# Performance work log

Hardware: AMD Instinct MI355X
Metric: run time of the kernel (lower is better)

Reference implementation:

```python
import jax, jax.numpy as jnp
import numpy as np

B, S, E, H, L, F, V = 8, 1024, 768, 12, 6, 3072, 32000
HD = E // H  # head_dim = 64
EPS = 1e-5


def _pos_encoding(max_len, dim):
    pos = np.arange(max_len, dtype=np.float32)[:, None]
    div = np.exp(np.arange(0, dim, 2, dtype=np.float32) * (-np.log(10000.0) / dim))
    pe = np.zeros((max_len, dim), dtype=np.float32)
    pe[:, 0::2] = np.sin(pos * div)
    pe[:, 1::2] = np.cos(pos * div)
    return jnp.asarray(pe)


def setup_inputs() -> dict:
    key = jax.random.key(0)
    ks = jax.random.split(key, 16)
    sd = 0.02
    inp = {}
    inp['input_ids'] = jax.random.randint(ks[0], (B, S), 0, V)
    inp['attention_mask'] = jnp.ones((B, S), dtype=jnp.int32)
    inp['emb'] = jax.random.normal(ks[1], (V, E), jnp.float32) * sd
    inp['pe'] = _pos_encoding(S, E)
    inp['Wq'] = jax.random.normal(ks[2], (L, E, E), jnp.float32) * sd
    inp['bq'] = jnp.zeros((L, E), jnp.float32)
    inp['Wk'] = jax.random.normal(ks[3], (L, E, E), jnp.float32) * sd
    inp['bk'] = jnp.zeros((L, E), jnp.float32)
    inp['Wv'] = jax.random.normal(ks[4], (L, E, E), jnp.float32) * sd
    inp['bv'] = jnp.zeros((L, E), jnp.float32)
    inp['Wo'] = jax.random.normal(ks[5], (L, E, E), jnp.float32) * sd
    inp['bo'] = jnp.zeros((L, E), jnp.float32)
    inp['ln1_g'] = jnp.ones((L, E), jnp.float32)
    inp['ln1_b'] = jnp.zeros((L, E), jnp.float32)
    inp['W1'] = jax.random.normal(ks[6], (L, E, F), jnp.float32) * sd
    inp['b1'] = jnp.zeros((L, F), jnp.float32)
    inp['W2'] = jax.random.normal(ks[7], (L, F, E), jnp.float32) * sd
    inp['b2'] = jnp.zeros((L, E), jnp.float32)
    inp['ln2_g'] = jnp.ones((L, E), jnp.float32)
    inp['ln2_b'] = jnp.zeros((L, E), jnp.float32)
    inp['Wc'] = jax.random.normal(ks[8], (E, 2), jnp.float32) * sd
    inp['bc'] = jnp.zeros((2,), jnp.float32)
    return inp


def _layernorm(x, g, b):
    mu = jnp.mean(x, axis=-1, keepdims=True)
    var = jnp.mean(jnp.square(x - mu), axis=-1, keepdims=True)
    return (x - mu) * jax.lax.rsqrt(var + EPS) * g + b


def reference(input_ids, attention_mask, emb, pe, Wq, bq, Wk, bk, Wv, bv, Wo, bo,
              ln1_g, ln1_b, W1, b1, W2, b2, ln2_g, ln2_b, Wc, bc):
    x = emb[input_ids] + pe[None, :S, :]           # [B,S,E] (dropout = eval identity)
    mask = attention_mask[:, None, None, :]        # [B,1,1,S]
    scale = jnp.sqrt(jnp.float32(HD))

    def block(x, p):
        wq, bq_, wk, bk_, wv, bv_, wo, bo_, g1, be1, w1, b1_, w2, b2_, g2, be2 = p
        q = (x @ wq + bq_).reshape(B, S, H, HD).transpose(0, 2, 1, 3)  # [B,H,S,D]
        k = (x @ wk + bk_).reshape(B, S, H, HD).transpose(0, 2, 1, 3)
        v = (x @ wv + bv_).reshape(B, S, H, HD).transpose(0, 2, 1, 3)
        scores = jnp.einsum('bhsd,bhtd->bhst', q, k) / scale          # [B,H,S,S]
        scores = jnp.where(mask == 0, -jnp.inf, scores)
        attn = jax.nn.softmax(scores, axis=-1)
        o = jnp.einsum('bhst,bhtd->bhsd', attn, v)
        o = o.transpose(0, 2, 1, 3).reshape(B, S, E) @ wo + bo_
        x = _layernorm(x + o, g1, be1)
        ffn = jax.nn.relu(x @ w1 + b1_) @ w2 + b2_
        x = _layernorm(x + ffn, g2, be2)
        return x, None

    params = (Wq, bq, Wk, bk, Wv, bv, Wo, bo, ln1_g, ln1_b, W1, b1, W2, b2, ln2_g, ln2_b)
    x, _ = jax.lax.scan(block, x, params)
    pooled = jnp.mean(x, axis=1)                   # [B,E]
    return pooled @ Wc + bc                        # [B,2]
```

## Files before the change

### kernel.cpp

```cpp
#include <hip/hip_runtime.h>

typedef __bf16 bf16x8 __attribute__((ext_vector_type(8)));
typedef float  f32x4  __attribute__((ext_vector_type(4)));

constexpr int Bb = 8, Ss = 1024, Ee = 768, Hh = 12, Ll = 6, Ff = 3072;
constexpr int TOK  = Bb * Ss;
constexpr int NQKV = 3 * Ee;

static __device__ __forceinline__ f32x4 mfma16(bf16x8 a, bf16x8 b, f32x4 c) {
  return __builtin_amdgcn_mfma_f32_16x16x32_bf16(a, b, c, 0, 0, 0);
}

static __device__ __forceinline__ void async16(const void* g, void* l) {
  __builtin_amdgcn_global_load_lds(
      (const __attribute__((address_space(1))) unsigned int*)g,
      (__attribute__((address_space(3))) unsigned int*)l, 16, 0, 0);
}

static __device__ __forceinline__ bf16x8 ds_read128(const __bf16* p) {
  bf16x8 r;
  unsigned a = (unsigned)(size_t)p;
  asm volatile("ds_read_b128 %0, %1" : "=v"(r) : "v"(a));
  return r;
}

static __device__ __forceinline__ float fexp2(float x) {
  float r; asm("v_exp_f32 %0, %1" : "=v"(r) : "v"(x)); return r;
}

__global__ __launch_bounds__(256) void embed_kernel(
    const int* __restrict__ ids, const float* __restrict__ emb,
    const float* __restrict__ pe, float* __restrict__ x, __bf16* __restrict__ xb)
{
  int tok = blockIdx.x;
  int s   = tok & (Ss - 1);
  int id  = ids[tok];
  const float* er = emb + (size_t)id * Ee;
  const float* pr = pe  + (size_t)s  * Ee;
  size_t base = (size_t)tok * Ee;
#pragma unroll
  for (int i = 0; i < 3; i++) {
    int e = threadIdx.x + i * 256;
    float v = er[e] + pr[e];
    x[base + e]  = v;
    xb[base + e] = (__bf16)v;
  }
}

__global__ __launch_bounds__(256) void transpose_w_kernel(
    const float* __restrict__ src, __bf16* __restrict__ dst,
    int K, int N, size_t sls, size_t dls)
{
  __shared__ float t[32][33];
  src += (size_t)blockIdx.z * sls;
  dst += (size_t)blockIdx.z * dls;
  int n0 = blockIdx.x * 32, k0 = blockIdx.y * 32;
  int c = threadIdx.x & 31, r0 = threadIdx.x >> 5;
#pragma unroll
  for (int rr = 0; rr < 32; rr += 8)
    t[r0 + rr][c] = src[(size_t)(k0 + r0 + rr) * N + n0 + c];
  __syncthreads();
#pragma unroll
  for (int rr = 0; rr < 32; rr += 8)
    dst[(size_t)(n0 + r0 + rr) * K + k0 + c] = (__bf16)t[c][r0 + rr];
}

template<bool OUT_BF16, bool RELU>
__global__ __launch_bounds__(256, 3) void gemm_kernel(
    const __bf16* __restrict__ A, const __bf16* __restrict__ Bt,
    const float* __restrict__ bias0, const float* __restrict__ bias1,
    const float* __restrict__ bias2, int bseg,
    float* __restrict__ Cf, __bf16* __restrict__ Cb, int M, int N, int K)
{
  __shared__ __align__(16) __bf16 lA[3][64 * 64];
  __shared__ __align__(16) __bf16 lB[3][64 * 64];
  const int tid  = threadIdx.x;
  const int wave = tid >> 6, lane = tid & 63;
  const int quad = lane >> 4, c16 = lane & 15;
  const int wm = wave >> 1, wn = wave & 1;

  const int bid = blockIdx.x;
  const int xcd = bid & 7;
  const int lb  = bid >> 3;
  const int mb  = xcd * 8 + (lb & 7);
  const int nb  = lb >> 3;
  const size_t m0 = (size_t)mb * 128, n0 = (size_t)nb * 128;

  f32x4 acc[4][4] = {};

  const int s0l = tid >> 3;
  const int s0c = tid & 7;
  const int l0  = s0c ^ (s0l & 7);
  const int tr0 = (s0l << 1) | (l0 >> 2);
  const int gc0 = (l0 & 3) * 8;
  const int s1l = (tid + 256) >> 3;
  const int l1  = s0c ^ (s1l & 7);
  const int tr1 = (s1l << 1) | (l1 >> 2);
  const int gc1 = (l1 & 3) * 8;

  const __bf16* Ag0 = A  + (m0 + tr0) * K + gc0;
  const __bf16* Ag1 = A  + (m0 + tr1) * K + gc1;
  const __bf16* Bg0 = Bt + (n0 + tr0) * K + gc0;
  const __bf16* Bg1 = Bt + (n0 + tr1) * K + gc1;
  const int d0 = tid * 8;

  const int nk = K >> 5;

  auto stage = [&](int t, int slot) {
    const int kof = t << 5;
    async16(Ag0 + kof, &lA[slot][d0]);
    async16(Ag1 + kof, &lA[slot][d0 + 2048]);
    async16(Bg0 + kof, &lB[slot][d0]);
    async16(Bg1 + kof, &lB[slot][d0 + 2048]);
  };

  int aoff[4], boff[4];
#pragma unroll
  for (int f = 0; f < 4; f++) {
    int ra = wm * 64 + f * 16 + c16;
    int ja = ra >> 1;
    aoff[f] = ja * 64 + (((((ra & 1) << 2) | quad)) ^ (ja & 7)) * 8;
    int rb = wn * 64 + f * 16 + c16;
    int jb = rb >> 1;
    boff[f] = jb * 64 + (((((rb & 1) << 2) | quad)) ^ (jb & 7)) * 8;
  }

  stage(0, 0);
  stage(1, 1);
  asm volatile("s_waitcnt vmcnt(4)" ::: "memory");
  __builtin_amdgcn_s_barrier();
  __builtin_amdgcn_sched_barrier(0);

  int slot = 0;
  for (int t = 0; t < nk; ++t) {
    if (t + 2 < nk) {
      int ns = slot + 2; if (ns >= 3) ns -= 3;
      stage(t + 2, ns);
    }
    const __bf16* la = &lA[slot][0];
    const __bf16* lb = &lB[slot][0];
    bf16x8 af[4], bfr[4];
#pragma unroll
    for (int f = 0; f < 4; f++) af[f]  = ds_read128(la + aoff[f]);
#pragma unroll
    for (int f = 0; f < 4; f++) bfr[f] = ds_read128(lb + boff[f]);
    asm volatile("s_waitcnt lgkmcnt(0)" ::: "memory");
    __builtin_amdgcn_sched_barrier(0);
    __builtin_amdgcn_s_setprio(1);
#pragma unroll
    for (int mi = 0; mi < 4; mi++)
#pragma unroll
      for (int ni = 0; ni < 4; ni++)
        acc[mi][ni] = mfma16(af[mi], bfr[ni], acc[mi][ni]);
    __builtin_amdgcn_s_setprio(0);
    __builtin_amdgcn_sched_barrier(0);
    if (t + 2 < nk) asm volatile("s_waitcnt vmcnt(4)" ::: "memory");
    else            asm volatile("s_waitcnt vmcnt(0)" ::: "memory");
    __builtin_amdgcn_s_barrier();
    __builtin_amdgcn_sched_barrier(0);
    slot = (slot + 1 == 3) ? 0 : slot + 1;
  }

#pragma unroll
  for (int ni = 0; ni < 4; ni++) {
    int col = (int)n0 + wn * 64 + ni * 16 + c16;
    const float* bp = bias0;
    int cc = col;
    if (cc >= bseg) { bp = bias1; cc -= bseg; }
    if (cc >= bseg) { bp = bias2; cc -= bseg; }
    float bv = bp[cc];
#pragma unroll
    for (int mi = 0; mi < 4; mi++) {
#pragma unroll
      for (int rr = 0; rr < 4; rr++) {
        size_t row = m0 + wm * 64 + mi * 16 + quad * 4 + rr;
        float v = acc[mi][ni][rr] + bv;
        if (RELU) v = fmaxf(v, 0.f);
        if (OUT_BF16) Cb[row * N + col] = (__bf16)v;
        else          Cf[row * N + col] = v;
      }
    }
  }
}

template<bool RELU>
__global__ __launch_bounds__(256, 2) void gemm_big_kernel(
    const __bf16* __restrict__ A, const __bf16* __restrict__ Bt,
    const float* __restrict__ bias0, const float* __restrict__ bias1,
    const float* __restrict__ bias2, int bseg,
    __bf16* __restrict__ Cb, int N, int K)
{
  __shared__ __align__(16) __bf16 lA[3][128 * 64];
  __shared__ __align__(16) __bf16 lB[3][64 * 64];
  const int tid  = threadIdx.x;
  const int wave = tid >> 6, lane = tid & 63;
  const int quad = lane >> 4, c16 = lane & 15;
  const int wm = wave >> 1, wn = wave & 1;

  const int bid = blockIdx.x;
  const int xcd = bid & 7;
  const int lb  = bid >> 3;
  const int mb  = xcd * 4 + (lb & 3);
  const int nb  = lb >> 2;
  const size_t m0 = (size_t)mb * 256, n0 = (size_t)nb * 128;

  f32x4 acc[8][4] = {};

  const __bf16* Agp[4];
#pragma unroll
  for (int j = 0; j < 4; j++) {
    int s = tid + j * 256, lr = s >> 3, sc = s & 7;
    int l = sc ^ (lr & 7);
    int tr = (lr << 1) | (l >> 2), gc = (l & 3) * 8;
    Agp[j] = A + (m0 + tr) * (size_t)K + gc;
  }
  const __bf16* Bgp[2];
#pragma unroll
  for (int j = 0; j < 2; j++) {
    int s = tid + j * 256, lr = s >> 3, sc = s & 7;
    int l = sc ^ (lr & 7);
    int tr = (lr << 1) | (l >> 2), gc = (l & 3) * 8;
    Bgp[j] = Bt + (n0 + tr) * (size_t)K + gc;
  }
  const int d0 = tid * 8;

  const int nk = K >> 5;

  auto stage = [&](int t, int slot) {
    const int kof = t << 5;
#pragma unroll
    for (int j = 0; j < 4; j++)
      async16(Agp[j] + kof, &lA[slot][d0 + j * 2048]);
#pragma unroll
    for (int j = 0; j < 2; j++)
      async16(Bgp[j] + kof, &lB[slot][d0 + j * 2048]);
  };

  int aoff[8], boff[4];
#pragma unroll
  for (int f = 0; f < 8; f++) {
    int ra = wm * 128 + f * 16 + c16;
    int ja = ra >> 1;
    aoff[f] = ja * 64 + ((((ra & 1) << 2) | quad) ^ (ja & 7)) * 8;
  }
#pragma unroll
  for (int f = 0; f < 4; f++) {
    int rb = wn * 64 + f * 16 + c16;
    int jb = rb >> 1;
    boff[f] = jb * 64 + ((((rb & 1) << 2) | quad) ^ (jb & 7)) * 8;
  }

  stage(0, 0);
  stage(1, 1);
  asm volatile("s_waitcnt vmcnt(6)" ::: "memory");
  __builtin_amdgcn_s_barrier();
  __builtin_amdgcn_sched_barrier(0);

  int slot = 0;
  for (int t = 0; t < nk; ++t) {
    if (t + 2 < nk) {
      int ns = slot + 2; if (ns >= 3) ns -= 3;
      stage(t + 2, ns);
    }
    const __bf16* la  = &lA[slot][0];
    const __bf16* lbp = &lB[slot][0];
    bf16x8 af[8], bfr[4];
#pragma unroll
    for (int f = 0; f < 8; f++) af[f]  = ds_read128(la + aoff[f]);
#pragma unroll
    for (int f = 0; f < 4; f++) bfr[f] = ds_read128(lbp + boff[f]);
    asm volatile("s_waitcnt lgkmcnt(0)" ::: "memory");
    __builtin_amdgcn_sched_barrier(0);
    __builtin_amdgcn_s_setprio(1);
#pragma unroll
    for (int mi = 0; mi < 8; mi++)
#pragma unroll
      for (int ni = 0; ni < 4; ni++)
        acc[mi][ni] = mfma16(af[mi], bfr[ni], acc[mi][ni]);
    __builtin_amdgcn_s_setprio(0);
    __builtin_amdgcn_sched_barrier(0);
    if (t + 2 < nk) asm volatile("s_waitcnt vmcnt(6)" ::: "memory");
    else            asm volatile("s_waitcnt vmcnt(0)" ::: "memory");
    __builtin_amdgcn_s_barrier();
    __builtin_amdgcn_sched_barrier(0);
    slot = (slot + 1 == 3) ? 0 : slot + 1;
  }

#pragma unroll
  for (int ni = 0; ni < 4; ni++) {
    int col = (int)n0 + wn * 64 + ni * 16 + c16;
    const float* bp = bias0;
    int cc = col;
    if (cc >= bseg) { bp = bias1; cc -= bseg; }
    if (cc >= bseg) { bp = bias2; cc -= bseg; }
    float bv = bp[cc];
#pragma unroll
    for (int mi = 0; mi < 8; mi++) {
#pragma unroll
      for (int rr = 0; rr < 4; rr++) {
        size_t row = m0 + wm * 128 + mi * 16 + quad * 4 + rr;
        float v = acc[mi][ni][rr] + bv;
        if (RELU) v = fmaxf(v, 0.f);
        Cb[row * N + col] = (__bf16)v;
      }
    }
  }
}

__global__ __launch_bounds__(256) void vtrans_kernel(
    const __bf16* __restrict__ qkv, __bf16* __restrict__ vt)
{
  int tid  = blockIdx.x * 256 + threadIdx.x;
  int d    = tid & 63;
  int rest = tid >> 6;
  int sc   = rest & 127;
  int bh   = rest >> 7;
  int b = bh / Hh, h = bh % Hh;
  const __bf16* src = qkv + (size_t)(b * Ss + sc * 8) * NQKV + 2 * Ee + h * 64 + d;
  bf16x8 v;
#pragma unroll
  for (int i = 0; i < 8; i++) v[i] = src[(size_t)i * NQKV];
  *(bf16x8*)(vt + ((size_t)bh * 64 + d) * Ss + sc * 8) = v;
}

__global__ __launch_bounds__(512, 6) void attn_kernel(
    const __bf16* __restrict__ qkv, const __bf16* __restrict__ vt,
    const int* __restrict__ amask, __bf16* __restrict__ out)
{
  __shared__ __align__(16) __bf16 kbuf[2][64 * 64];
  __shared__ __align__(16) __bf16 vbuf[2][64 * 64];
  __shared__ __align__(16) __bf16 plds[8][16 * 68];
  const int idx = blockIdx.x;
  const int bh = idx % 96, qi = idx / 96;
  const int b = bh / Hh, h = bh % Hh;
  const int lane = threadIdx.x & 63, wave = threadIdx.x >> 6;
  const int quad = lane >> 4, c16 = lane & 15;
  const int q0 = qi * 128 + wave * 16;

  const __bf16* qbase = qkv + (size_t)(b * Ss + q0 + c16) * NQKV + h * 64 + quad * 8;
  bf16x8 qf0 = *(const bf16x8*)(qbase);
  bf16x8 qf1 = *(const bf16x8*)(qbase + 32);

  const int srow = threadIdx.x >> 3;
  const int scol = ((threadIdx.x & 7) ^ (srow & 7)) * 8;
  const __bf16* kg = qkv + (size_t)(b * Ss + srow) * NQKV + Ee + h * 64 + scol;
  const __bf16* vg = vt + ((size_t)bh * 64 + srow) * Ss + scol;

  const int sa8 = c16 & 7;
  const int rc0 = (quad ^ sa8) * 8;
  const int rc1 = ((quad + 4) ^ sa8) * 8;

  f32x4 o[4] = {};
  float lrow[4] = {0.f, 0.f, 0.f, 0.f};
  const int* mp = amask + b * Ss;
  __bf16* pw = &plds[wave][0];
  const float CE = 0.18033688f;

  async16(kg, &kbuf[0][(size_t)threadIdx.x * 8]);
  async16(vg, &vbuf[0][(size_t)threadIdx.x * 8]);

  for (int t = 0; t < 16; t++) {
    const int tb = t * 64;
    __syncthreads();
    if (t < 15) {
      const int nb = (t + 1) & 1, ntb = tb + 64;
      async16(kg + (size_t)ntb * NQKV, &kbuf[nb][(size_t)threadIdx.x * 8]);
      async16(vg + ntb,                &vbuf[nb][(size_t)threadIdx.x * 8]);
    }
    const __bf16* kb = &kbuf[t & 1][0];
    const __bf16* vb = &vbuf[t & 1][0];

    float mk2[4];
#pragma unroll
    for (int n = 0; n < 4; n++) mk2[n] = mp[tb + n * 16 + c16] ? 0.f : -1e30f;
    bf16x8 kf[8], vf[8];
#pragma unroll
    for (int n = 0; n < 4; n++) {
      kf[2*n]   = *(const bf16x8*)(kb + (n * 16 + c16) * 64 + rc0);
      kf[2*n+1] = *(const bf16x8*)(kb + (n * 16 + c16) * 64 + rc1);
    }
#pragma unroll
    for (int n = 0; n < 4; n++) {
      vf[2*n]   = *(const bf16x8*)(vb + (n * 16 + c16) * 64 + rc0);
      vf[2*n+1] = *(const bf16x8*)(vb + (n * 16 + c16) * 64 + rc1);
    }

    f32x4 s[4];
#pragma unroll
    for (int n = 0; n < 4; n++) {
      f32x4 z = {};
      z = mfma16(qf0, kf[2*n], z);
      s[n] = mfma16(qf1, kf[2*n+1], z);
    }

#pragma unroll
    for (int rr = 0; rr < 4; rr++) {
      float p0 = fexp2(fmaf(s[0][rr], CE, mk2[0]));
      float p1 = fexp2(fmaf(s[1][rr], CE, mk2[1]));
      float p2 = fexp2(fmaf(s[2][rr], CE, mk2[2]));
      float p3 = fexp2(fmaf(s[3][rr], CE, mk2[3]));
      lrow[rr] += (p0 + p1) + (p2 + p3);
      int prow = (quad * 4 + rr) * 68;
      pw[prow + 0  + c16] = (__bf16)p0;
      pw[prow + 16 + c16] = (__bf16)p1;
      pw[prow + 32 + c16] = (__bf16)p2;
      pw[prow + 48 + c16] = (__bf16)p3;
    }

    bf16x8 pf0 = *(const bf16x8*)(pw + c16 * 68 + quad * 8);
    bf16x8 pf1 = *(const bf16x8*)(pw + c16 * 68 + 32 + quad * 8);
#pragma unroll
    for (int ni = 0; ni < 4; ni++) {
      o[ni] = mfma16(pf0, vf[2*ni],   o[ni]);
      o[ni] = mfma16(pf1, vf[2*ni+1], o[ni]);
    }
  }

#pragma unroll
  for (int rr = 0; rr < 4; rr++) {
    float sr = lrow[rr];
    sr += __shfl_xor(sr, 1);
    sr += __shfl_xor(sr, 2);
    sr += __shfl_xor(sr, 4);
    sr += __shfl_xor(sr, 8);
    float inv = 1.f / sr;
    size_t row = (size_t)(b * Ss + q0 + quad * 4 + rr) * Ee + h * 64;
    out[row + 0  + c16] = (__bf16)(o[0][rr] * inv);
    out[row + 16 + c16] = (__bf16)(o[1][rr] * inv);
    out[row + 32 + c16] = (__bf16)(o[2][rr] * inv);
    out[row + 48 + c16] = (__bf16)(o[3][rr] * inv);
  }
}

__global__ __launch_bounds__(256) void add_ln_kernel(
    const float* __restrict__ xin, const float* __restrict__ tmp,
    const float* __restrict__ g, const float* __restrict__ beta,
    float* __restrict__ xout, __bf16* __restrict__ xbout)
{
  __shared__ float red[8];
  size_t base = (size_t)blockIdx.x * Ee;
  float hv[3], s = 0.f, sq = 0.f;
#pragma unroll
  for (int i = 0; i < 3; i++) {
    int e = threadIdx.x + i * 256;
    hv[i] = xin[base + e] + tmp[base + e];
    s += hv[i]; sq += hv[i] * hv[i];
  }
#pragma unroll
  for (int m = 1; m < 64; m <<= 1) { s += __shfl_xor(s, m); sq += __shfl_xor(sq, m); }
  int wave = threadIdx.x >> 6;
  if ((threadIdx.x & 63) == 0) { red[wave] = s; red[4 + wave] = sq; }
  __syncthreads();
  s  = red[0] + red[1] + red[2] + red[3];
  sq = red[4] + red[5] + red[6] + red[7];
  float mean = s * (1.f / Ee);
  float var  = sq * (1.f / Ee) - mean * mean;
  float rstd = rsqrtf(var + 1e-5f);
#pragma unroll
  for (int i = 0; i < 3; i++) {
    int e = threadIdx.x + i * 256;
    float v = (hv[i] - mean) * rstd * g[e] + beta[e];
    xout[base + e]  = v;
    xbout[base + e] = (__bf16)v;
  }
}

__global__ __launch_bounds__(256) void pool1_kernel(
    const float* __restrict__ x, float* __restrict__ partial)
{
  int b = blockIdx.x, chunk = blockIdx.y;
  float acc[3] = {0.f, 0.f, 0.f};
  for (int s = chunk * 64; s < chunk * 64 + 64; s++) {
#pragma unroll
    for (int i = 0; i < 3; i++) {
      int e = threadIdx.x + i * 256;
      acc[i] += x[((size_t)b * Ss + s) * Ee + e];
    }
  }
#pragma unroll
  for (int i = 0; i < 3; i++) {
    int e = threadIdx.x + i * 256;
    partial[((size_t)b * 16 + chunk) * Ee + e] = acc[i];
  }
}

__global__ __launch_bounds__(256) void pool2_kernel(
    const float* __restrict__ partial, const float* __restrict__ Wc,
    const float* __restrict__ bc, float* __restrict__ out)
{
  __shared__ float red[8];
  int b = blockIdx.x;
  float p0 = 0.f, p1 = 0.f;
#pragma unroll
  for (int i = 0; i < 3; i++) {
    int e = threadIdx.x + i * 256;
    float pe_ = 0.f;
#pragma unroll
    for (int c = 0; c < 16; c++) pe_ += partial[((size_t)b * 16 + c) * Ee + e];
    pe_ *= (1.f / Ss);
    p0 += pe_ * Wc[e * 2 + 0];
    p1 += pe_ * Wc[e * 2 + 1];
  }
#pragma unroll
  for (int m = 1; m < 64; m <<= 1) { p0 += __shfl_xor(p0, m); p1 += __shfl_xor(p1, m); }
  int wave = threadIdx.x >> 6;
  if ((threadIdx.x & 63) == 0) { red[wave] = p0; red[4 + wave] = p1; }
  __syncthreads();
  if (threadIdx.x == 0) {
    out[b * 2 + 0] = red[0] + red[1] + red[2] + red[3] + bc[0];
    out[b * 2 + 1] = red[4] + red[5] + red[6] + red[7] + bc[1];
  }
}

extern "C" void kernel_launch(void* const* d_in, const int* in_sizes, int n_in,
                              void* d_out, int out_size, void* d_ws, size_t ws_size,
                              hipStream_t stream) {
  const int*   ids   = (const int*)  d_in[0];
  const int*   amask = (const int*)  d_in[1];
  const float* emb   = (const float*)d_in[2];
  const float* pe    = (const float*)d_in[3];
  const float* Wq    = (const float*)d_in[4];
  const float* bq    = (const float*)d_in[5];
  const float* Wk    = (const float*)d_in[6];
  const float* bk    = (const float*)d_in[7];
  const float* Wv    = (const float*)d_in[8];
  const float* bv    = (const float*)d_in[9];
  const float* Wo    = (const float*)d_in[10];
  const float* bo    = (const float*)d_in[11];
  const float* ln1g  = (const float*)d_in[12];
  const float* ln1b  = (const float*)d_in[13];
  const float* W1    = (const float*)d_in[14];
  const float* b1    = (const float*)d_in[15];
  const float* W2    = (const float*)d_in[16];
  const float* b2    = (const float*)d_in[17];
  const float* ln2g  = (const float*)d_in[18];
  const float* ln2b  = (const float*)d_in[19];
  const float* Wc    = (const float*)d_in[20];
  const float* bc    = (const float*)d_in[21];
  float* outp = (float*)d_out;

  char* p = (char*)d_ws;
  auto alloc = [&](size_t bytes) { char* r = p; p += (bytes + 255) & ~(size_t)255; return r; };
  float*  x     = (float*) alloc((size_t)TOK * Ee * 4);
  __bf16* xb    = (__bf16*)alloc((size_t)TOK * Ee * 2);
  float*  tmp   = (float*) alloc((size_t)TOK * Ee * 4);
  __bf16* attn  = (__bf16*)alloc((size_t)TOK * Ee * 2);
  char*   r1    = alloc((size_t)TOK * Ff * 2);
  __bf16* qkv   = (__bf16*)r1;
  __bf16* vt    = (__bf16*)(r1 + (size_t)TOK * NQKV * 2);
  __bf16* h1    = (__bf16*)r1;
  __bf16* wqkvt = (__bf16*)alloc((size_t)Ll * NQKV * Ee * 2);
  __bf16* wot   = (__bf16*)alloc((size_t)Ll * Ee * Ee * 2);
  __bf16* w1t   = (__bf16*)alloc((size_t)Ll * Ff * Ee * 2);
  __bf16* w2t   = (__bf16*)alloc((size_t)Ll * Ee * Ff * 2);
  float*  part  = (float*) alloc((size_t)Bb * 16 * Ee * 4);

  embed_kernel<<<TOK, 256, 0, stream>>>(ids, emb, pe, x, xb);

  transpose_w_kernel<<<dim3(Ee/32, Ee/32, Ll), 256, 0, stream>>>(
      Wq, wqkvt,                         Ee, Ee, (size_t)Ee*Ee, (size_t)NQKV*Ee);
  transpose_w_kernel<<<dim3(Ee/32, Ee/32, Ll), 256, 0, stream>>>(
      Wk, wqkvt + (size_t)Ee*Ee,         Ee, Ee, (size_t)Ee*Ee, (size_t)NQKV*Ee);
  transpose_w_kernel<<<dim3(Ee/32, Ee/32, Ll), 256, 0, stream>>>(
      Wv, wqkvt + (size_t)2*Ee*Ee,       Ee, Ee, (size_t)Ee*Ee, (size_t)NQKV*Ee);
  transpose_w_kernel<<<dim3(Ee/32, Ee/32, Ll), 256, 0, stream>>>(
      Wo, wot,                           Ee, Ee, (size_t)Ee*Ee, (size_t)Ee*Ee);
  transpose_w_kernel<<<dim3(Ff/32, Ee/32, Ll), 256, 0, stream>>>(
      W1, w1t,                           Ee, Ff, (size_t)Ee*Ff, (size_t)Ff*Ee);
  transpose_w_kernel<<<dim3(Ee/32, Ff/32, Ll), 256, 0, stream>>>(
      W2, w2t,                           Ff, Ee, (size_t)Ff*Ee, (size_t)Ee*Ff);

  for (int l = 0; l < Ll; l++) {
    gemm_big_kernel<false><<<8 * 4 * (NQKV/128), 256, 0, stream>>>(
        xb, wqkvt + (size_t)l*NQKV*Ee,
        bq + l*Ee, bk + l*Ee, bv + l*Ee, Ee,
        qkv, NQKV, Ee);
    vtrans_kernel<<<3072, 256, 0, stream>>>(qkv, vt);
    attn_kernel<<<768, 512, 0, stream>>>(qkv, vt, amask, attn);
    gemm_kernel<false, false><<<64 * (Ee/128), 256, 0, stream>>>(
        attn, wot + (size_t)l*Ee*Ee,
        bo + l*Ee, bo + l*Ee, bo + l*Ee, Ee,
        tmp, nullptr, TOK, Ee, Ee);
    add_ln_kernel<<<TOK, 256, 0, stream>>>(x, tmp, ln1g + l*Ee, ln1b + l*Ee, x, xb);
    gemm_big_kernel<true><<<8 * 4 * (Ff/128), 256, 0, stream>>>(
        xb, w1t + (size_t)l*Ff*Ee,
        b1 + l*Ff, b1 + l*Ff, b1 + l*Ff, Ff,
        h1, Ff, Ee);
    gemm_kernel<false, false><<<64 * (Ee/128), 256, 0, stream>>>(
        h1, w2t + (size_t)l*Ee*Ff,
        b2 + l*Ee, b2 + l*Ee, b2 + l*Ee, Ee,
        tmp, nullptr, TOK, Ee, Ff);
    add_ln_kernel<<<TOK, 256, 0, stream>>>(x, tmp, ln2g + l*Ee, ln2b + l*Ee, x, xb);
  }

  pool1_kernel<<<dim3(Bb, 16), 256, 0, stream>>>(x, part);
  pool2_kernel<<<Bb, 256, 0, stream>>>(part, Wc, bc, outp);
}
```

Measured before the change: 1.928 ms.

## Replace big-tile GEMM with 64-row tile kernel for N=768 projections

New measurement: 1.989 ms. 3.2% more time.

```diff
diff --git a/kernel.cpp b/kernel.cpp
--- a/kernel.cpp
+++ b/kernel.cpp
@@ -183,76 +183,70 @@
   }
 }
 
-template<bool RELU>
-__global__ __launch_bounds__(256, 2) void gemm_big_kernel(
+__global__ __launch_bounds__(256, 4) void gemm64_kernel(
     const __bf16* __restrict__ A, const __bf16* __restrict__ Bt,
-    const float* __restrict__ bias0, const float* __restrict__ bias1,
-    const float* __restrict__ bias2, int bseg,
-    __bf16* __restrict__ Cb, int N, int K)
-{
-  __shared__ __align__(16) __bf16 lA[3][128 * 64];
+    const float* __restrict__ bias0,
+    float* __restrict__ Cf, int N, int K)
+{
+  __shared__ __align__(16) __bf16 lA[3][32 * 64];
   __shared__ __align__(16) __bf16 lB[3][64 * 64];
   const int tid  = threadIdx.x;
-  const int wave = tid >> 6, lane = tid & 63;
+  const int lane = tid & 63, wn = tid >> 6;
   const int quad = lane >> 4, c16 = lane & 15;
-  const int wm = wave >> 1, wn = wave & 1;
 
   const int bid = blockIdx.x;
   const int xcd = bid & 7;
   const int lb  = bid >> 3;
-  const int mb  = xcd * 4 + (lb & 3);
-  const int nb  = lb >> 2;
-  const size_t m0 = (size_t)mb * 256, n0 = (size_t)nb * 128;
-
-  f32x4 acc[8][4] = {};
-
-  const __bf16* Agp[4];
-#pragma unroll
-  for (int j = 0; j < 4; j++) {
-    int s = tid + j * 256, lr = s >> 3, sc = s & 7;
-    int l = sc ^ (lr & 7);
-    int tr = (lr << 1) | (l >> 2), gc = (l & 3) * 8;
-    Agp[j] = A + (m0 + tr) * (size_t)K + gc;
-  }
-  const __bf16* Bgp[2];
-#pragma unroll
-  for (int j = 0; j < 2; j++) {
-    int s = tid + j * 256, lr = s >> 3, sc = s & 7;
-    int l = sc ^ (lr & 7);
-    int tr = (lr << 1) | (l >> 2), gc = (l & 3) * 8;
-    Bgp[j] = Bt + (n0 + tr) * (size_t)K + gc;
-  }
+  const int mb  = xcd * 16 + (lb & 15);
+  const int nb  = lb >> 4;
+  const size_t m0 = (size_t)mb * 64, n0 = (size_t)nb * 128;
+
+  f32x4 acc[4][2] = {};
+
+  const int alr = tid >> 3, asc = tid & 7;
+  const int al  = asc ^ (alr & 7);
+  const int atr = (alr << 1) | (al >> 2);
+  const int agc = (al & 3) * 8;
+  const __bf16* Ag = A + (m0 + atr) * (size_t)K + agc;
+  const int s0l = tid >> 3;
+  const int s0c = tid & 7;
+  const int l0  = s0c ^ (s0l & 7);
+  const int tr0 = (s0l << 1) | (l0 >> 2);
+  const int gc0 = (l0 & 3) * 8;
+  const int s1l = (tid + 256) >> 3;
+  const int l1  = s0c ^ (s1l & 7);
+  const int tr1 = (s1l << 1) | (l1 >> 2);
+  const int gc1 = (l1 & 3) * 8;
+  const __bf16* Bg0 = Bt + (n0 + tr0) * (size_t)K + gc0;
+  const __bf16* Bg1 = Bt + (n0 + tr1) * (size_t)K + gc1;
   const int d0 = tid * 8;
 
   const int nk = K >> 5;
 
   auto stage = [&](int t, int slot) {
     const int kof = t << 5;
-#pragma unroll
-    for (int j = 0; j < 4; j++)
-      async16(Agp[j] + kof, &lA[slot][d0 + j * 2048]);
-#pragma unroll
-    for (int j = 0; j < 2; j++)
-      async16(Bgp[j] + kof, &lB[slot][d0 + j * 2048]);
+    async16(Ag  + kof, &lA[slot][d0]);
+    async16(Bg0 + kof, &lB[slot][d0]);
+    async16(Bg1 + kof, &lB[slot][d0 + 2048]);
   };
 
-  int aoff[8], boff[4];
-#pragma unroll
-  for (int f = 0; f < 8; f++) {
-    int ra = wm * 128 + f * 16 + c16;
+  int aoff[4], boff[2];
+#pragma unroll
+  for (int f = 0; f < 4; f++) {
+    int ra = f * 16 + c16;
     int ja = ra >> 1;
     aoff[f] = ja * 64 + ((((ra & 1) << 2) | quad) ^ (ja & 7)) * 8;
   }
 #pragma unroll
-  for (int f = 0; f < 4; f++) {
-    int rb = wn * 64 + f * 16 + c16;
+  for (int f = 0; f < 2; f++) {
+    int rb = wn * 32 + f * 16 + c16;
     int jb = rb >> 1;
     boff[f] = jb * 64 + ((((rb & 1) << 2) | quad) ^ (jb & 7)) * 8;
   }
 
   stage(0, 0);
   stage(1, 1);
-  asm volatile("s_waitcnt vmcnt(6)" ::: "memory");
+  asm volatile("s_waitcnt vmcnt(3)" ::: "memory");
   __builtin_amdgcn_s_barrier();
   __builtin_amdgcn_sched_barrier(0);
 
@@ -262,24 +256,24 @@
       int ns = slot + 2; if (ns >= 3) ns -= 3;
       stage(t + 2, ns);
     }
-    const __bf16* la  = &lA[slot][0];
-    const __bf16* lbp = &lB[slot][0];
-    bf16x8 af[8], bfr[4];
-#pragma unroll
-    for (int f = 0; f < 8; f++) af[f]  = ds_read128(la + aoff[f]);
-#pragma unroll
-    for (int f = 0; f < 4; f++) bfr[f] = ds_read128(lbp + boff[f]);
+    const __bf16* la = &lA[slot][0];
+    const __bf16* lb = &lB[slot][0];
+    bf16x8 af[4], bfr[2];
+#pragma unroll
+    for (int f = 0; f < 4; f++) af[f]  = ds_read128(la + aoff[f]);
+#pragma unroll
+    for (int f = 0; f < 2; f++) bfr[f] = ds_read128(lb + boff[f]);
     asm volatile("s_waitcnt lgkmcnt(0)" ::: "memory");
     __builtin_amdgcn_sched_barrier(0);
     __builtin_amdgcn_s_setprio(1);
 #pragma unroll
-    for (int mi = 0; mi < 8; mi++)
-#pragma unroll
-      for (int ni = 0; ni < 4; ni++)
+    for (int mi = 0; mi < 4; mi++)
+#pragma unroll
+      for (int ni = 0; ni < 2; ni++)
         acc[mi][ni] = mfma16(af[mi], bfr[ni], acc[mi][ni]);
     __builtin_amdgcn_s_setprio(0);
     __builtin_amdgcn_sched_barrier(0);
-    if (t + 2 < nk) asm volatile("s_waitcnt vmcnt(6)" ::: "memory");
+    if (t + 2 < nk) asm volatile("s_waitcnt vmcnt(3)" ::: "memory");
     else            asm volatile("s_waitcnt vmcnt(0)" ::: "memory");
     __builtin_amdgcn_s_barrier();
     __builtin_amdgcn_sched_barrier(0);
@@ -287,21 +281,15 @@
   }
 
 #pragma unroll
-  for (int ni = 0; ni < 4; ni++) {
-    int col = (int)n0 + wn * 64 + ni * 16 + c16;
-    const float* bp = bias0;
-    int cc = col;
-    if (cc >= bseg) { bp = bias1; cc -= bseg; }
-    if (cc >= bseg) { bp = bias2; cc -= bseg; }
-    float bv = bp[cc];
-#pragma unroll
-    for (int mi = 0; mi < 8; mi++) {
+  for (int ni = 0; ni < 2; ni++) {
+    int col = (int)n0 + wn * 32 + ni * 16 + c16;
+    float bv = bias0[col];
+#pragma unroll
+    for (int mi = 0; mi < 4; mi++) {
 #pragma unroll
       for (int rr = 0; rr < 4; rr++) {
-        size_t row = m0 + wm * 128 + mi * 16 + quad * 4 + rr;
-        float v = acc[mi][ni][rr] + bv;
-        if (RELU) v = fmaxf(v, 0.f);
-        Cb[row * N + col] = (__bf16)v;
+        size_t row = m0 + mi * 16 + quad * 4 + rr;
+        Cf[row * N + col] = acc[mi][ni][rr] + bv;
       }
     }
   }
@@ -571,25 +559,21 @@
       W2, w2t,                           Ff, Ee, (size_t)Ff*Ee, (size_t)Ee*Ff);
 
   for (int l = 0; l < Ll; l++) {
-    gemm_big_kernel<false><<<8 * 4 * (NQKV/128), 256, 0, stream>>>(
+    gemm_kernel<true, false><<<64 * (NQKV/128), 256, 0, stream>>>(
         xb, wqkvt + (size_t)l*NQKV*Ee,
         bq + l*Ee, bk + l*Ee, bv + l*Ee, Ee,
-        qkv, NQKV, Ee);
+        nullptr, qkv, TOK, NQKV, Ee);
     vtrans_kernel<<<3072, 256, 0, stream>>>(qkv, vt);
     attn_kernel<<<768, 512, 0, stream>>>(qkv, vt, amask, attn);
-    gemm_kernel<false, false><<<64 * (Ee/128), 256, 0, stream>>>(
-        attn, wot + (size_t)l*Ee*Ee,
-        bo + l*Ee, bo + l*Ee, bo + l*Ee, Ee,
-        tmp, nullptr, TOK, Ee, Ee);
+    gemm64_kernel<<<768, 256, 0, stream>>>(
+        attn, wot + (size_t)l*Ee*Ee, bo + l*Ee, tmp, Ee, Ee);
     add_ln_kernel<<<TOK, 256, 0, stream>>>(x, tmp, ln1g + l*Ee, ln1b + l*Ee, x, xb);
-    gemm_big_kernel<true><<<8 * 4 * (Ff/128), 256, 0, stream>>>(
+    gemm_kernel<true, true><<<64 * (Ff/128), 256, 0, stream>>>(
         xb, w1t + (size_t)l*Ff*Ee,
         b1 + l*Ff, b1 + l*Ff, b1 + l*Ff, Ff,
-        h1, Ff, Ee);
-    gemm_kernel<false, false><<<64 * (Ee/128), 256, 0, stream>>>(
-        h1, w2t + (size_t)l*Ee*Ff,
-        b2 + l*Ee, b2 + l*Ee, b2 + l*Ee, Ee,
-        tmp, nullptr, TOK, Ee, Ff);
+        nullptr, h1, TOK, Ff, Ee);
+    gemm64_kernel<<<768, 256, 0, stream>>>(
+        h1, w2t + (size_t)l*Ee*Ff, b2 + l*Ee, tmp, Ee, Ff);
     add_ln_kernel<<<TOK, 256, 0, stream>>>(x, tmp, ln2g + l*Ee, ln2b + l*Ee, x, xb);
   }
 
```
